# Performance work log

Measured on AMD Instinct MI355X. Metric: run time of the kernel, lower is better.

## Reference

```python
import jax, jax.numpy as jnp
import numpy as np
from jax import lax

SHARED = 512
THRESH = 1.0   # LifNeuron threshold from source
DECAY = 0.9    # assumed LIF membrane decay (LifNeuron source not provided)


def spike(u):
    return (u >= 0.0).astype(u.dtype)


def lif(x):
    # Leaky integrate-and-fire over the time axis. x: (B, T, D) -> spikes (B, T, D)
    def step(mem, xt):
        mem = DECAY * mem + xt
        s = spike(mem - THRESH)
        return mem - s * THRESH, s
    x_t = jnp.swapaxes(x, 0, 1)  # (T, B, D)
    _, spikes = lax.scan(step, jnp.zeros((x.shape[0], x.shape[2]), x.dtype), x_t)
    return jnp.swapaxes(spikes, 0, 1)


def setup_inputs() -> dict:
    key = jax.random.key(0)
    ks = jax.random.split(key, 10)
    B, T, S = 2, 32, 64
    Dv, Da = 768, 512
    TENSOR_DIM = (SHARED + 1) ** 2  # 263169

    def lin_w(k, fan_in, fan_out):
        # torch.nn.Linear default init scale ~ 1/sqrt(fan_in)
        return (jax.random.normal(k, (fan_out, fan_in), jnp.float32)
                * np.float32(1.0 / np.sqrt(fan_in)))

    return {
        "vision": jax.random.uniform(ks[0], (B, T, S, Dv), jnp.float32),
        "audio": jax.random.uniform(ks[1], (B, T, S, Da), jnp.float32),
        "vw1": lin_w(ks[2], Dv, SHARED), "vb1": jnp.zeros((SHARED,), jnp.float32),
        "vw2": lin_w(ks[3], SHARED, SHARED), "vb2": jnp.zeros((SHARED,), jnp.float32),
        "aw1": lin_w(ks[4], Da, SHARED), "ab1": jnp.zeros((SHARED,), jnp.float32),
        "aw2": lin_w(ks[5], SHARED, SHARED), "ab2": jnp.zeros((SHARED,), jnp.float32),
        "fw1": lin_w(ks[6], TENSOR_DIM, 2 * SHARED), "fb1": jnp.zeros((2 * SHARED,), jnp.float32),
        "fw2": lin_w(ks[7], 2 * SHARED, SHARED), "fb2": jnp.zeros((SHARED,), jnp.float32),
    }


def reference(vision, audio, vw1, vb1, vw2, vb2, aw1, ab1, aw2, ab2,
              fw1, fb1, fw2, fb2):
    def unimodal(x, w1, b1, w2, b2):
        p = x.mean(axis=2)  # (B, T, D_mod) - pool over spike/token axis
        h = jax.nn.relu(jnp.einsum('btd,hd->bth', p, w1) + b1)
        h = jnp.einsum('bth,oh->bto', h, w2) + b2  # (B, T, SHARED)
        ones = jnp.ones(h.shape[:-1] + (1,), h.dtype)
        return jnp.concatenate([h, ones], axis=-1)  # (B, T, SHARED+1)

    a = unimodal(vision, vw1, vb1, vw2, vb2)
    b = unimodal(audio, aw1, ab1, aw2, ab2)
    B, T, _ = a.shape
    # outer-product tensor fusion: (B, T, (SHARED+1)^2)
    tp = jnp.einsum('btd,bte->btde', a, b).reshape(B, T, -1)
    h = jax.nn.relu(jnp.einsum('btk,ok->bto', tp, fw1) + fb1)
    fused = jnp.einsum('bto,fo->btf', h, fw2) + fb2  # (B, T, SHARED)
    return lif(fused)
```

## Files before the change

kernel.cpp:

```cpp
#include <hip/hip_runtime.h>

#define AB 513
#define TD 263169

typedef float f4 __attribute__((ext_vector_type(4)));
typedef float f32x4 __attribute__((ext_vector_type(4)));
typedef short bf16x8 __attribute__((ext_vector_type(8)));
typedef int i32x4 __attribute__((ext_vector_type(4)));
#define GAS __attribute__((address_space(1)))
#define LAS __attribute__((address_space(3)))

__global__ __launch_bounds__(256) void pool_kernel(
    const float* __restrict__ vx, const float* __restrict__ ax,
    float* __restrict__ pvT, float* __restrict__ paT)
{
    int b = blockIdx.x;
    const float* x; float* pT; int D, bt, dc;
    if (b < 192) { x = vx; pT = pvT; D = 768; bt = b / 3; dc = b % 3; }
    else { b -= 192; x = ax; pT = paT; D = 512; bt = b >> 1; dc = b & 1; }
    const int d = dc * 256 + threadIdx.x;
    const float* xp = x + (size_t)bt * 64 * D + d;
    float s0 = 0.f, s1 = 0.f, s2 = 0.f, s3 = 0.f;
    #pragma unroll 4
    for (int ss = 0; ss < 64; ss += 4) {
        s0 += xp[(size_t)ss * D];
        s1 += xp[(size_t)(ss + 1) * D];
        s2 += xp[(size_t)(ss + 2) * D];
        s3 += xp[(size_t)(ss + 3) * D];
    }
    pT[d * 64 + bt] = ((s0 + s1) + (s2 + s3)) * 0.015625f;
}

__global__ __launch_bounds__(512) void mlp1_kernel(
    const float* __restrict__ pvT, const float* __restrict__ paT,
    const float* __restrict__ vw1, const float* __restrict__ vb1,
    const float* __restrict__ aw1, const float* __restrict__ ab1,
    float* __restrict__ h1vT, float* __restrict__ h1aT)
{
    const int isA = (blockIdx.x >= 64);
    const int D = isA ? 512 : 768;
    const float* pT = isA ? paT : pvT;
    const float* w1 = isA ? aw1 : vw1;
    const float* b1 = isA ? ab1 : vb1;
    float* h1T = isA ? h1aT : h1vT;
    const int tid = threadIdx.x, lane = tid & 63, w = tid >> 6;
    const int h = (blockIdx.x & 63) * 8 + w;
    const float* wr = w1 + (size_t)h * D;

    float a0 = 0.f, a1 = 0.f, a2 = 0.f, a3 = 0.f;
    for (int d = 0; d < D; d += 16) {
        const f4 w0 = *(const f4*)(wr + d);
        const f4 w1v = *(const f4*)(wr + d + 4);
        const f4 w2v = *(const f4*)(wr + d + 8);
        const f4 w3v = *(const f4*)(wr + d + 12);
        #pragma unroll
        for (int q = 0; q < 4; ++q) {
            a0 = fmaf(w0[q],  pT[(d + q) * 64 + lane], a0);
            a1 = fmaf(w1v[q], pT[(d + 4 + q) * 64 + lane], a1);
            a2 = fmaf(w2v[q], pT[(d + 8 + q) * 64 + lane], a2);
            a3 = fmaf(w3v[q], pT[(d + 12 + q) * 64 + lane], a3);
        }
    }
    h1T[h * 64 + lane] = fmaxf((a0 + a1) + (a2 + a3) + b1[h], 0.f);
}

__global__ __launch_bounds__(512) void mlp2_kernel(
    const float* __restrict__ h1vT, const float* __restrict__ h1aT,
    const float* __restrict__ vw2, const float* __restrict__ vb2,
    const float* __restrict__ aw2, const float* __restrict__ ab2,
    float* __restrict__ aTout, float* __restrict__ bTout)
{
    const int isA = (blockIdx.x >= 64);
    const float* hT = isA ? h1aT : h1vT;
    const float* w2 = isA ? aw2 : vw2;
    const float* b2 = isA ? ab2 : vb2;
    float* outT = isA ? bTout : aTout;
    const int tid = threadIdx.x, lane = tid & 63, w = tid >> 6;
    const int h = (blockIdx.x & 63) * 8 + w;
    const float* wr = w2 + (size_t)h * 512;

    float a0 = 0.f, a1 = 0.f, a2 = 0.f, a3 = 0.f;
    for (int d = 0; d < 512; d += 16) {
        const f4 w0 = *(const f4*)(wr + d);
        const f4 w1v = *(const f4*)(wr + d + 4);
        const f4 w2v = *(const f4*)(wr + d + 8);
        const f4 w3v = *(const f4*)(wr + d + 12);
        #pragma unroll
        for (int q = 0; q < 4; ++q) {
            a0 = fmaf(w0[q],  hT[(d + q) * 64 + lane], a0);
            a1 = fmaf(w1v[q], hT[(d + 4 + q) * 64 + lane], a1);
            a2 = fmaf(w2v[q], hT[(d + 8 + q) * 64 + lane], a2);
            a3 = fmaf(w3v[q], hT[(d + 12 + q) * 64 + lane], a3);
        }
    }
    outT[h * 64 + lane] = (a0 + a1) + (a2 + a3) + b2[h];
    if ((blockIdx.x & 63) == 0 && tid < 64) outT[512 * 64 + tid] = 1.0f;
}

__global__ __launch_bounds__(256) void aprep_kernel(
    const float* __restrict__ aT,
    short* __restrict__ aFc)
{
    const int t = blockIdx.x * 256 + threadIdx.x;
    const int l = t & 63, mt = (t >> 6) & 3, kt = t >> 8;
    const int m = mt * 16 + (l & 15);
    const int kbase = kt * 32 + ((l >> 4) << 3);
    const int cb = kt * 12 + mt * 3;
    #pragma unroll
    for (int i = 0; i < 8; ++i) {
        const float v = aT[(size_t)(kbase + i) * 64 + m];
        const unsigned u = __float_as_uint(v);
        const float r1 = v - __uint_as_float(u & 0xFFFF0000u);
        const unsigned u1 = __float_as_uint(r1);
        const float r2 = r1 - __uint_as_float(u1 & 0xFFFF0000u);
        const unsigned u2 = __float_as_uint(r2);
        aFc[((size_t)(cb + 0) * 64 + l) * 8 + i] = (short)(u >> 16);
        aFc[((size_t)(cb + 1) * 64 + l) * 8 + i] = (short)(u1 >> 16);
        aFc[((size_t)(cb + 2) * 64 + l) * 8 + i] = (short)(u2 >> 16);
    }
}

__global__ __launch_bounds__(512, 1) void bilinear_kernel(
    const float* __restrict__ fw1,
    const float* __restrict__ fb1,
    const float* __restrict__ aT,
    const float* __restrict__ bT,
    const short* __restrict__ aFc,
    float* __restrict__ hbufT)
{
    __shared__ float wring[3][8192];
    __shared__ short aring[3][6144];
    __shared__ float adump[256];

    const int tid = threadIdx.x;
    const int l = tid & 63, w = tid >> 6;
    const int o = blockIdx.x;
    const float* __restrict__ W = fw1 + (size_t)o * TD;
    const int lq = l >> 4, ln = l & 15;

    #define STAGE_W(e_)                                                        \
        do {                                                                   \
            const int ee_ = (e_), kt_ = ee_ >> 1, eh_ = ee_ & 1, en_ = ee_ % 3;\
            _Pragma("unroll")                                                  \
            for (int rr_ = 0; rr_ < 4; ++rr_) {                                \
                const int r_ = w * 4 + rr_;                                    \
                __builtin_amdgcn_global_load_lds(                              \
                    (const GAS unsigned*)(const void*)(W + (size_t)(kt_ * 32 + r_) * AB + 256 * eh_ + l * 4), \
                    (LAS unsigned*)(void*)(&wring[en_][r_ * 256]), 16, 0, 0);  \
            }                                                                  \
        } while (0)

    #define STAGE_A(kt_)                                                       \
        do {                                                                   \
            const int kk_ = (kt_), en_ = kk_ % 3;                              \
            const int c0_ = (w < 4) ? (2 * w) : (4 + w);                       \
            const short* s0_ = aFc + ((size_t)kk_ * 12 + c0_) * 512;           \
            __builtin_amdgcn_global_load_lds(                                  \
                (const GAS unsigned*)(const void*)(s0_ + l * 8),               \
                (LAS unsigned*)(void*)(&aring[en_][c0_ * 512]), 16, 0, 0);     \
            if (w < 4) {                                                       \
                const int c1_ = 2 * w + 1;                                     \
                const short* s1_ = aFc + ((size_t)kk_ * 12 + c1_) * 512;       \
                __builtin_amdgcn_global_load_lds(                              \
                    (const GAS unsigned*)(const void*)(s1_ + l * 8),           \
                    (LAS unsigned*)(void*)(&aring[en_][c1_ * 512]), 16, 0, 0); \
            } else {                                                           \
                const short* s1_ = aFc + (size_t)kk_ * 12 * 512;               \
                __builtin_amdgcn_global_load_lds(                              \
                    (const GAS unsigned*)(const void*)(s1_ + l * 2),           \
                    (LAS unsigned*)(void*)(adump), 4, 0, 0);                   \
            }                                                                  \
        } while (0)

    #define LOADA_LDS(kt_)                                                     \
        do {                                                                   \
            const int en_ = (kt_) % 3;                                         \
            _Pragma("unroll")                                                  \
            for (int mt_ = 0; mt_ < 4; ++mt_) {                                \
                A1[mt_] = *(const bf16x8*)&aring[en_][(mt_ * 3 + 0) * 512 + l * 8]; \
                A2[mt_] = *(const bf16x8*)&aring[en_][(mt_ * 3 + 1) * 512 + l * 8]; \
                A3[mt_] = *(const bf16x8*)&aring[en_][(mt_ * 3 + 2) * 512 + l * 8]; \
            }                                                                  \
        } while (0)

    #define COMPUTE(e_, EHC)                                                   \
        do {                                                                   \
            const float* __restrict__ wb_ = &wring[(e_) % 3][0];               \
            _Pragma("unroll")                                                  \
            for (int ntl = 0; ntl < 2; ++ntl) {                                \
                const int col_ = 32 * w + 16 * ntl + ln;                       \
                unsigned u0[8], u1[8], u2[8];                                  \
                _Pragma("unroll")                                              \
                for (int i = 0; i < 8; ++i) {                                  \
                    const float v = wb_[(lq * 8 + i) * 256 + col_];            \
                    u0[i] = __float_as_uint(v);                                \
                    const float r1 = v - __uint_as_float(u0[i] & 0xFFFF0000u); \
                    u1[i] = __float_as_uint(r1);                               \
                    const float r2 = r1 - __uint_as_float(u1[i] & 0xFFFF0000u);\
                    u2[i] = __float_as_uint(r2);                               \
                }                                                              \
                i32x4 p1, p2, p3;                                              \
                _Pragma("unroll")                                              \
                for (int j = 0; j < 4; ++j) {                                  \
                    p1[j] = (int)((u0[2 * j + 1] & 0xFFFF0000u) | (u0[2 * j] >> 16)); \
                    p2[j] = (int)((u1[2 * j + 1] & 0xFFFF0000u) | (u1[2 * j] >> 16)); \
                    p3[j] = (int)((u2[2 * j + 1] & 0xFFFF0000u) | (u2[2 * j] >> 16)); \
                }                                                              \
                const bf16x8 B1 = __builtin_bit_cast(bf16x8, p1);              \
                const bf16x8 B2 = __builtin_bit_cast(bf16x8, p2);              \
                const bf16x8 B3 = __builtin_bit_cast(bf16x8, p3);              \
                _Pragma("unroll")                                              \
                for (int mt = 0; mt < 4; ++mt) {                               \
                    acc[mt][(EHC) * 2 + ntl] = __builtin_amdgcn_mfma_f32_16x16x32_bf16(A1[mt], B1, acc[mt][(EHC) * 2 + ntl], 0, 0, 0); \
                    acc[mt][(EHC) * 2 + ntl] = __builtin_amdgcn_mfma_f32_16x16x32_bf16(A1[mt], B2, acc[mt][(EHC) * 2 + ntl], 0, 0, 0); \
                    acc[mt][(EHC) * 2 + ntl] = __builtin_amdgcn_mfma_f32_16x16x32_bf16(A2[mt], B1, acc[mt][(EHC) * 2 + ntl], 0, 0, 0); \
                    acc[mt][(EHC) * 2 + ntl] = __builtin_amdgcn_mfma_f32_16x16x32_bf16(A2[mt], B2, acc[mt][(EHC) * 2 + ntl], 0, 0, 0); \
                    acc[mt][(EHC) * 2 + ntl] = __builtin_amdgcn_mfma_f32_16x16x32_bf16(A1[mt], B3, acc[mt][(EHC) * 2 + ntl], 0, 0, 0); \
                    acc[mt][(EHC) * 2 + ntl] = __builtin_amdgcn_mfma_f32_16x16x32_bf16(A3[mt], B1, acc[mt][(EHC) * 2 + ntl], 0, 0, 0); \
                }                                                              \
            }                                                                  \
        } while (0)

    f32x4 acc[4][4];
    #pragma unroll
    for (int mt = 0; mt < 4; ++mt)
        #pragma unroll
        for (int nt = 0; nt < 4; ++nt)
            acc[mt][nt] = (f32x4){0.f, 0.f, 0.f, 0.f};
    bf16x8 A1[4], A2[4], A3[4];

    STAGE_W(0);
    STAGE_A(0);
    STAGE_W(1);
    STAGE_A(1);

    #pragma unroll 1
    for (int kt = 0; kt < 16; ++kt) {
        const int e0 = 2 * kt;
        asm volatile("s_waitcnt vmcnt(6)" ::: "memory");
        __builtin_amdgcn_s_barrier();
        LOADA_LDS(kt);
        COMPUTE(e0, 0);
        __builtin_amdgcn_s_barrier();
        STAGE_W(e0 + 2 <= 31 ? e0 + 2 : 31);
        STAGE_A(kt + 2 <= 15 ? kt + 2 : 15);
        asm volatile("s_waitcnt vmcnt(6)" ::: "memory");
        __builtin_amdgcn_s_barrier();
        COMPUTE(e0 + 1, 1);
        __builtin_amdgcn_s_barrier();
        STAGE_W(e0 + 3 <= 31 ? e0 + 3 : 31);
    }
    asm volatile("s_waitcnt vmcnt(0)" ::: "memory");
    __builtin_amdgcn_s_barrier();

    float ysum[4][4];
    #pragma unroll
    for (int mt = 0; mt < 4; ++mt)
        #pragma unroll
        for (int r = 0; r < 4; ++r) ysum[mt][r] = 0.f;
    #pragma unroll
    for (int mt = 0; mt < 4; ++mt) {
        const int bt0 = mt * 16 + lq * 4;
        #pragma unroll
        for (int ntg = 0; ntg < 4; ++ntg) {
            const int e = 256 * (ntg >> 1) + 32 * w + 16 * (ntg & 1) + ln;
            const f4 bv = *(const f4*)(bT + (size_t)e * 64 + bt0);
            #pragma unroll
            for (int r = 0; r < 4; ++r)
                ysum[mt][r] = fmaf(acc[mt][ntg][r], bv[r], ysum[mt][r]);
        }
    }
    #pragma unroll
    for (int mt = 0; mt < 4; ++mt)
        #pragma unroll
        for (int r = 0; r < 4; ++r) {
            float v = ysum[mt][r];
            v += __shfl_xor(v, 1, 64);
            v += __shfl_xor(v, 2, 64);
            v += __shfl_xor(v, 4, 64);
            v += __shfl_xor(v, 8, 64);
            ysum[mt][r] = v;
        }
    if (ln == 0) {
        #pragma unroll
        for (int mt = 0; mt < 4; ++mt)
            #pragma unroll
            for (int r = 0; r < 4; ++r)
                wring[0][w * 64 + mt * 16 + lq * 4 + r] = ysum[mt][r];
    }

    {
        const int we0 = w * 64;
        float s0 = 0.f, s1 = 0.f, s2 = 0.f, s3 = 0.f;
        #pragma unroll 4
        for (int k = 0; k < 64; k += 4) {
            s0 = fmaf(aT[(size_t)(we0 + k) * 64 + l], W[(size_t)(we0 + k) * AB + 512], s0);
            s1 = fmaf(aT[(size_t)(we0 + k + 1) * 64 + l], W[(size_t)(we0 + k + 1) * AB + 512], s1);
            s2 = fmaf(aT[(size_t)(we0 + k + 2) * 64 + l], W[(size_t)(we0 + k + 2) * AB + 512], s2);
            s3 = fmaf(aT[(size_t)(we0 + k + 3) * 64 + l], W[(size_t)(we0 + k + 3) * AB + 512], s3);
        }
        #pragma unroll 4
        for (int k = 0; k < 64; k += 4) {
            s0 = fmaf(W[(size_t)512 * AB + we0 + k], bT[(size_t)(we0 + k) * 64 + l], s0);
            s1 = fmaf(W[(size_t)512 * AB + we0 + k + 1], bT[(size_t)(we0 + k + 1) * 64 + l], s1);
            s2 = fmaf(W[(size_t)512 * AB + we0 + k + 2], bT[(size_t)(we0 + k + 2) * 64 + l], s2);
            s3 = fmaf(W[(size_t)512 * AB + we0 + k + 3], bT[(size_t)(we0 + k + 3) * 64 + l], s3);
        }
        wring[0][512 + w * 64 + l] = (s0 + s1) + (s2 + s3);
    }

    __syncthreads();

    if (w == 0) {
        float t2 = 0.f;
        #pragma unroll
        for (int k = 0; k < 8; ++k)
            t2 += wring[0][k * 64 + l] + wring[0][512 + k * 64 + l];
        t2 += W[(size_t)512 * AB + 512] + fb1[o];
        hbufT[(size_t)o * 64 + l] = fmaxf(t2, 0.f);
    }
    #undef STAGE_W
    #undef STAGE_A
    #undef LOADA_LDS
    #undef COMPUTE
}

__global__ __launch_bounds__(512) void fuse2_kernel(
    const float* __restrict__ hbufT,
    const float* __restrict__ fw2,
    const float* __restrict__ fb2,
    float* __restrict__ fused)
{
    const int tid = threadIdx.x, lane = tid & 63, w = tid >> 6;
    #pragma unroll
    for (int k = 0; k < 2; ++k) {
        const int f = blockIdx.x * 16 + w * 2 + k;
        const float* wr = fw2 + (size_t)f * 1024;
        float a0 = 0.f, a1 = 0.f, a2 = 0.f, a3 = 0.f;
        for (int o = 0; o < 1024; o += 16) {
            const f4 w0 = *(const f4*)(wr + o);
            const f4 w1v = *(const f4*)(wr + o + 4);
            const f4 w2v = *(const f4*)(wr + o + 8);
            const f4 w3v = *(const f4*)(wr + o + 12);
            #pragma unroll
            for (int q = 0; q < 4; ++q) {
                a0 = fmaf(w0[q],  hbufT[(o + q) * 64 + lane], a0);
                a1 = fmaf(w1v[q], hbufT[(o + 4 + q) * 64 + lane], a1);
                a2 = fmaf(w2v[q], hbufT[(o + 8 + q) * 64 + lane], a2);
                a3 = fmaf(w3v[q], hbufT[(o + 12 + q) * 64 + lane], a3);
            }
        }
        fused[lane * 512 + f] = (a0 + a1) + (a2 + a3) + fb2[f];
    }
}

__global__ __launch_bounds__(256) void lif_kernel(
    const float* __restrict__ fused,
    float* __restrict__ out)
{
    const int idx = blockIdx.x * 256 + threadIdx.x;
    if (idx >= 1024) return;
    const int b = idx >> 9, dd = idx & 511;
    float mem = 0.f;
    for (int t = 0; t < 32; ++t) {
        const size_t off = ((size_t)(b * 32 + t) * 512) + dd;
        mem = 0.9f * mem + fused[off];
        const float s = (mem >= 1.0f) ? 1.0f : 0.0f;
        out[off] = s;
        mem -= s;
    }
}

extern "C" void kernel_launch(void* const* d_in, const int* in_sizes, int n_in,
                              void* d_out, int out_size, void* d_ws, size_t ws_size,
                              hipStream_t stream) {
    const float* vision = (const float*)d_in[0];
    const float* audio  = (const float*)d_in[1];
    const float* vw1 = (const float*)d_in[2];
    const float* vb1 = (const float*)d_in[3];
    const float* vw2 = (const float*)d_in[4];
    const float* vb2 = (const float*)d_in[5];
    const float* aw1 = (const float*)d_in[6];
    const float* ab1 = (const float*)d_in[7];
    const float* aw2 = (const float*)d_in[8];
    const float* ab2 = (const float*)d_in[9];
    const float* fw1 = (const float*)d_in[10];
    const float* fb1 = (const float*)d_in[11];
    const float* fw2 = (const float*)d_in[12];
    const float* fb2 = (const float*)d_in[13];
    float* out = (float*)d_out;

    float* ws    = (float*)d_ws;
    float* pvT   = ws;
    float* paT   = pvT + 768 * 64;
    float* h1vT  = paT + 512 * 64;
    float* h1aT  = h1vT + 512 * 64;
    float* aT    = h1aT + 512 * 64;
    float* bT    = aT + AB * 64;
    float* hbufT = bT + AB * 64;
    float* fused = hbufT + 1024 * 64;
    short* aFc   = (short*)(fused + 64 * 512);

    pool_kernel<<<320, 256, 0, stream>>>(vision, audio, pvT, paT);
    mlp1_kernel<<<128, 512, 0, stream>>>(pvT, paT, vw1, vb1, aw1, ab1, h1vT, h1aT);
    mlp2_kernel<<<128, 512, 0, stream>>>(h1vT, h1aT, vw2, vb2, aw2, ab2, aT, bT);
    aprep_kernel<<<16, 256, 0, stream>>>(aT, aFc);
    bilinear_kernel<<<1024, 512, 0, stream>>>(fw1, fb1, aT, bT, aFc, hbufT);
    fuse2_kernel<<<32, 512, 0, stream>>>(hbufT, fw2, fb2, fused);
    lif_kernel<<<4, 256, 0, stream>>>(fused, out);
}
```

Before: 440.8 us.

## Swap bilinear GEMM operand roles and load fw1 directly into registers

The bilinear kernel now treats the fw1 rows as the MFMA A operand and the precomputed bf16-split b vectors as B, instead of the reverse. Each wave loads its own 64 rows of fw1 straight from global memory into registers with a two-register double buffer. This replaces the LDS ring, global_load_lds staging and barriers. The final contraction with a also folds in the column-512 weight term. The change removes LDS traffic and barrier synchronisation, but the fw1 reads are now strided row accesses (8 floats per lane across rows of stride 513), which may coalesce poorly, and register pressure rises.

```diff
diff --git a/kernel.cpp b/kernel.cpp
--- a/kernel.cpp
+++ b/kernel.cpp
@@ -7,8 +7,6 @@
 typedef float f32x4 __attribute__((ext_vector_type(4)));
 typedef short bf16x8 __attribute__((ext_vector_type(8)));
 typedef int i32x4 __attribute__((ext_vector_type(4)));
-#define GAS __attribute__((address_space(1)))
-#define LAS __attribute__((address_space(3)))
 
 __global__ __launch_bounds__(256) void pool_kernel(
     const float* __restrict__ vx, const float* __restrict__ ax,
@@ -97,26 +95,26 @@
     if ((blockIdx.x & 63) == 0 && tid < 64) outT[512 * 64 + tid] = 1.0f;
 }
 
-__global__ __launch_bounds__(256) void aprep_kernel(
-    const float* __restrict__ aT,
-    short* __restrict__ aFc)
+__global__ __launch_bounds__(256) void bprep_kernel(
+    const float* __restrict__ bT,
+    short* __restrict__ bF)
 {
     const int t = blockIdx.x * 256 + threadIdx.x;
-    const int l = t & 63, mt = (t >> 6) & 3, kt = t >> 8;
-    const int m = mt * 16 + (l & 15);
-    const int kbase = kt * 32 + ((l >> 4) << 3);
-    const int cb = kt * 12 + mt * 3;
+    const int l = t & 63, frag = t >> 6;
+    const int kt = frag / 12, rem = frag % 12;
+    const int nt = rem / 3, lvl = rem % 3;
+    const int bt = nt * 16 + (l & 15);
+    const int ebase = kt * 32 + ((l >> 4) << 3);
     #pragma unroll
     for (int i = 0; i < 8; ++i) {
-        const float v = aT[(size_t)(kbase + i) * 64 + m];
+        const float v = bT[(size_t)(ebase + i) * 64 + bt];
         const unsigned u = __float_as_uint(v);
         const float r1 = v - __uint_as_float(u & 0xFFFF0000u);
         const unsigned u1 = __float_as_uint(r1);
         const float r2 = r1 - __uint_as_float(u1 & 0xFFFF0000u);
         const unsigned u2 = __float_as_uint(r2);
-        aFc[((size_t)(cb + 0) * 64 + l) * 8 + i] = (short)(u >> 16);
-        aFc[((size_t)(cb + 1) * 64 + l) * 8 + i] = (short)(u1 >> 16);
-        aFc[((size_t)(cb + 2) * 64 + l) * 8 + i] = (short)(u2 >> 16);
+        const unsigned sel = (lvl == 0) ? u : (lvl == 1) ? u1 : u2;
+        bF[(size_t)frag * 512 + l * 8 + i] = (short)(sel >> 16);
     }
 }
 
@@ -125,74 +123,48 @@
     const float* __restrict__ fb1,
     const float* __restrict__ aT,
     const float* __restrict__ bT,
-    const short* __restrict__ aFc,
+    const short* __restrict__ bF,
     float* __restrict__ hbufT)
 {
-    __shared__ float wring[3][8192];
-    __shared__ short aring[3][6144];
-    __shared__ float adump[256];
+    __shared__ float red[8][64];
+    __shared__ float redB[8][64];
 
     const int tid = threadIdx.x;
     const int l = tid & 63, w = tid >> 6;
     const int o = blockIdx.x;
     const float* __restrict__ W = fw1 + (size_t)o * TD;
-    const int lq = l >> 4, ln = l & 15;
-
-    #define STAGE_W(e_)                                                        \
+    const int ln = l & 15, lq = l >> 4;
+
+    #define WLOAD(W0r, W1r, kt_)                                               \
         do {                                                                   \
-            const int ee_ = (e_), kt_ = ee_ >> 1, eh_ = ee_ & 1, en_ = ee_ % 3;\
             _Pragma("unroll")                                                  \
-            for (int rr_ = 0; rr_ < 4; ++rr_) {                                \
-                const int r_ = w * 4 + rr_;                                    \
-                __builtin_amdgcn_global_load_lds(                              \
-                    (const GAS unsigned*)(const void*)(W + (size_t)(kt_ * 32 + r_) * AB + 256 * eh_ + l * 4), \
-                    (LAS unsigned*)(void*)(&wring[en_][r_ * 256]), 16, 0, 0);  \
+            for (int mt_ = 0; mt_ < 4; ++mt_) {                                \
+                const float* p_ = W + (size_t)((w * 4 + mt_) * 16 + ln) * AB   \
+                                    + (kt_) * 32 + lq * 8;                     \
+                W0r[mt_] = *(const f4*)p_;                                     \
+                W1r[mt_] = *(const f4*)(p_ + 4);                               \
             }                                                                  \
         } while (0)
 
-    #define STAGE_A(kt_)                                                       \
+    #define BLOAD(kt_)                                                         \
         do {                                                                   \
-            const int kk_ = (kt_), en_ = kk_ % 3;                              \
-            const int c0_ = (w < 4) ? (2 * w) : (4 + w);                       \
-            const short* s0_ = aFc + ((size_t)kk_ * 12 + c0_) * 512;           \
-            __builtin_amdgcn_global_load_lds(                                  \
-                (const GAS unsigned*)(const void*)(s0_ + l * 8),               \
-                (LAS unsigned*)(void*)(&aring[en_][c0_ * 512]), 16, 0, 0);     \
-            if (w < 4) {                                                       \
-                const int c1_ = 2 * w + 1;                                     \
-                const short* s1_ = aFc + ((size_t)kk_ * 12 + c1_) * 512;       \
-                __builtin_amdgcn_global_load_lds(                              \
-                    (const GAS unsigned*)(const void*)(s1_ + l * 8),           \
-                    (LAS unsigned*)(void*)(&aring[en_][c1_ * 512]), 16, 0, 0); \
-            } else {                                                           \
-                const short* s1_ = aFc + (size_t)kk_ * 12 * 512;               \
-                __builtin_amdgcn_global_load_lds(                              \
-                    (const GAS unsigned*)(const void*)(s1_ + l * 2),           \
-                    (LAS unsigned*)(void*)(adump), 4, 0, 0);                   \
+            _Pragma("unroll")                                                  \
+            for (int nt_ = 0; nt_ < 4; ++nt_) {                                \
+                const short* q_ = bF + (size_t)(((kt_) * 4 + nt_) * 3) * 512 + l * 8; \
+                B1[nt_] = *(const bf16x8*)(q_);                                \
+                B2[nt_] = *(const bf16x8*)(q_ + 512);                          \
+                B3[nt_] = *(const bf16x8*)(q_ + 1024);                         \
             }                                                                  \
         } while (0)
 
-    #define LOADA_LDS(kt_)                                                     \
+    #define COMPUTE(W0r, W1r)                                                  \
         do {                                                                   \
-            const int en_ = (kt_) % 3;                                         \
             _Pragma("unroll")                                                  \
-            for (int mt_ = 0; mt_ < 4; ++mt_) {                                \
-                A1[mt_] = *(const bf16x8*)&aring[en_][(mt_ * 3 + 0) * 512 + l * 8]; \
-                A2[mt_] = *(const bf16x8*)&aring[en_][(mt_ * 3 + 1) * 512 + l * 8]; \
-                A3[mt_] = *(const bf16x8*)&aring[en_][(mt_ * 3 + 2) * 512 + l * 8]; \
-            }                                                                  \
-        } while (0)
-
-    #define COMPUTE(e_, EHC)                                                   \
-        do {                                                                   \
-            const float* __restrict__ wb_ = &wring[(e_) % 3][0];               \
-            _Pragma("unroll")                                                  \
-            for (int ntl = 0; ntl < 2; ++ntl) {                                \
-                const int col_ = 32 * w + 16 * ntl + ln;                       \
+            for (int mt = 0; mt < 4; ++mt) {                                   \
                 unsigned u0[8], u1[8], u2[8];                                  \
                 _Pragma("unroll")                                              \
                 for (int i = 0; i < 8; ++i) {                                  \
-                    const float v = wb_[(lq * 8 + i) * 256 + col_];            \
+                    const float v = (i < 4) ? W0r[mt][i] : W1r[mt][i - 4];     \
                     u0[i] = __float_as_uint(v);                                \
                     const float r1 = v - __uint_as_float(u0[i] & 0xFFFF0000u); \
                     u1[i] = __float_as_uint(r1);                               \
@@ -206,17 +178,17 @@
                     p2[j] = (int)((u1[2 * j + 1] & 0xFFFF0000u) | (u1[2 * j] >> 16)); \
                     p3[j] = (int)((u2[2 * j + 1] & 0xFFFF0000u) | (u2[2 * j] >> 16)); \
                 }                                                              \
-                const bf16x8 B1 = __builtin_bit_cast(bf16x8, p1);              \
-                const bf16x8 B2 = __builtin_bit_cast(bf16x8, p2);              \
-                const bf16x8 B3 = __builtin_bit_cast(bf16x8, p3);              \
+                const bf16x8 A1 = __builtin_bit_cast(bf16x8, p1);              \
+                const bf16x8 A2 = __builtin_bit_cast(bf16x8, p2);              \
+                const bf16x8 A3 = __builtin_bit_cast(bf16x8, p3);              \
                 _Pragma("unroll")                                              \
-                for (int mt = 0; mt < 4; ++mt) {                               \
-                    acc[mt][(EHC) * 2 + ntl] = __builtin_amdgcn_mfma_f32_16x16x32_bf16(A1[mt], B1, acc[mt][(EHC) * 2 + ntl], 0, 0, 0); \
-                    acc[mt][(EHC) * 2 + ntl] = __builtin_amdgcn_mfma_f32_16x16x32_bf16(A1[mt], B2, acc[mt][(EHC) * 2 + ntl], 0, 0, 0); \
-                    acc[mt][(EHC) * 2 + ntl] = __builtin_amdgcn_mfma_f32_16x16x32_bf16(A2[mt], B1, acc[mt][(EHC) * 2 + ntl], 0, 0, 0); \
-                    acc[mt][(EHC) * 2 + ntl] = __builtin_amdgcn_mfma_f32_16x16x32_bf16(A2[mt], B2, acc[mt][(EHC) * 2 + ntl], 0, 0, 0); \
-                    acc[mt][(EHC) * 2 + ntl] = __builtin_amdgcn_mfma_f32_16x16x32_bf16(A1[mt], B3, acc[mt][(EHC) * 2 + ntl], 0, 0, 0); \
-                    acc[mt][(EHC) * 2 + ntl] = __builtin_amdgcn_mfma_f32_16x16x32_bf16(A3[mt], B1, acc[mt][(EHC) * 2 + ntl], 0, 0, 0); \
+                for (int nt = 0; nt < 4; ++nt) {                               \
+                    acc[mt][nt] = __builtin_amdgcn_mfma_f32_16x16x32_bf16(A1, B1[nt], acc[mt][nt], 0, 0, 0); \
+                    acc[mt][nt] = __builtin_amdgcn_mfma_f32_16x16x32_bf16(A1, B2[nt], acc[mt][nt], 0, 0, 0); \
+                    acc[mt][nt] = __builtin_amdgcn_mfma_f32_16x16x32_bf16(A2, B1[nt], acc[mt][nt], 0, 0, 0); \
+                    acc[mt][nt] = __builtin_amdgcn_mfma_f32_16x16x32_bf16(A2, B2[nt], acc[mt][nt], 0, 0, 0); \
+                    acc[mt][nt] = __builtin_amdgcn_mfma_f32_16x16x32_bf16(A1, B3[nt], acc[mt][nt], 0, 0, 0); \
+                    acc[mt][nt] = __builtin_amdgcn_mfma_f32_16x16x32_bf16(A3, B1[nt], acc[mt][nt], 0, 0, 0); \
                 }                                                              \
             }                                                                  \
         } while (0)
@@ -227,86 +199,65 @@
         #pragma unroll
         for (int nt = 0; nt < 4; ++nt)
             acc[mt][nt] = (f32x4){0.f, 0.f, 0.f, 0.f};
-    bf16x8 A1[4], A2[4], A3[4];
-
-    STAGE_W(0);
-    STAGE_A(0);
-    STAGE_W(1);
-    STAGE_A(1);
+
+    f4 Wa0[4], Wa1[4], Wb0[4], Wb1[4];
+    bf16x8 B1[4], B2[4], B3[4];
+
+    WLOAD(Wa0, Wa1, 0);
 
     #pragma unroll 1
-    for (int kt = 0; kt < 16; ++kt) {
-        const int e0 = 2 * kt;
-        asm volatile("s_waitcnt vmcnt(6)" ::: "memory");
-        __builtin_amdgcn_s_barrier();
-        LOADA_LDS(kt);
-        COMPUTE(e0, 0);
-        __builtin_amdgcn_s_barrier();
-        STAGE_W(e0 + 2 <= 31 ? e0 + 2 : 31);
-        STAGE_A(kt + 2 <= 15 ? kt + 2 : 15);
-        asm volatile("s_waitcnt vmcnt(6)" ::: "memory");
-        __builtin_amdgcn_s_barrier();
-        COMPUTE(e0 + 1, 1);
-        __builtin_amdgcn_s_barrier();
-        STAGE_W(e0 + 3 <= 31 ? e0 + 3 : 31);
-    }
-    asm volatile("s_waitcnt vmcnt(0)" ::: "memory");
-    __builtin_amdgcn_s_barrier();
-
-    float ysum[4][4];
-    #pragma unroll
-    for (int mt = 0; mt < 4; ++mt)
-        #pragma unroll
-        for (int r = 0; r < 4; ++r) ysum[mt][r] = 0.f;
+    for (int it = 0; it < 7; ++it) {
+        const int kt = 2 * it;
+        WLOAD(Wb0, Wb1, kt + 1);
+        BLOAD(kt);
+        COMPUTE(Wa0, Wa1);
+        WLOAD(Wa0, Wa1, kt + 2);
+        BLOAD(kt + 1);
+        COMPUTE(Wb0, Wb1);
+    }
+    WLOAD(Wb0, Wb1, 15);
+    BLOAD(14);
+    COMPUTE(Wa0, Wa1);
+    BLOAD(15);
+    COMPUTE(Wb0, Wb1);
+
+    float y[4] = {0.f, 0.f, 0.f, 0.f};
     #pragma unroll
     for (int mt = 0; mt < 4; ++mt) {
-        const int bt0 = mt * 16 + lq * 4;
-        #pragma unroll
-        for (int ntg = 0; ntg < 4; ++ntg) {
-            const int e = 256 * (ntg >> 1) + 32 * w + 16 * (ntg & 1) + ln;
-            const f4 bv = *(const f4*)(bT + (size_t)e * 64 + bt0);
+        #pragma unroll
+        for (int r = 0; r < 4; ++r) {
+            const int d = 64 * w + mt * 16 + lq * 4 + r;
+            const float wc = W[(size_t)d * AB + 512];
             #pragma unroll
-            for (int r = 0; r < 4; ++r)
-                ysum[mt][r] = fmaf(acc[mt][ntg][r], bv[r], ysum[mt][r]);
-        }
-    }
-    #pragma unroll
-    for (int mt = 0; mt < 4; ++mt)
-        #pragma unroll
-        for (int r = 0; r < 4; ++r) {
-            float v = ysum[mt][r];
-            v += __shfl_xor(v, 1, 64);
-            v += __shfl_xor(v, 2, 64);
-            v += __shfl_xor(v, 4, 64);
-            v += __shfl_xor(v, 8, 64);
-            ysum[mt][r] = v;
-        }
-    if (ln == 0) {
-        #pragma unroll
-        for (int mt = 0; mt < 4; ++mt)
-            #pragma unroll
-            for (int r = 0; r < 4; ++r)
-                wring[0][w * 64 + mt * 16 + lq * 4 + r] = ysum[mt][r];
+            for (int nt = 0; nt < 4; ++nt) {
+                const float av = aT[(size_t)d * 64 + nt * 16 + ln];
+                y[nt] = fmaf(av, acc[mt][nt][r] + wc, y[nt]);
+            }
+        }
+    }
+    #pragma unroll
+    for (int nt = 0; nt < 4; ++nt) {
+        float v = y[nt];
+        v += __shfl_xor(v, 16, 64);
+        v += __shfl_xor(v, 32, 64);
+        y[nt] = v;
+    }
+    if (lq == 0) {
+        #pragma unroll
+        for (int nt = 0; nt < 4; ++nt) red[w][nt * 16 + ln] = y[nt];
     }
 
     {
-        const int we0 = w * 64;
         float s0 = 0.f, s1 = 0.f, s2 = 0.f, s3 = 0.f;
+        const int e0 = 64 * w;
         #pragma unroll 4
         for (int k = 0; k < 64; k += 4) {
-            s0 = fmaf(aT[(size_t)(we0 + k) * 64 + l], W[(size_t)(we0 + k) * AB + 512], s0);
-            s1 = fmaf(aT[(size_t)(we0 + k + 1) * 64 + l], W[(size_t)(we0 + k + 1) * AB + 512], s1);
-            s2 = fmaf(aT[(size_t)(we0 + k + 2) * 64 + l], W[(size_t)(we0 + k + 2) * AB + 512], s2);
-            s3 = fmaf(aT[(size_t)(we0 + k + 3) * 64 + l], W[(size_t)(we0 + k + 3) * AB + 512], s3);
-        }
-        #pragma unroll 4
-        for (int k = 0; k < 64; k += 4) {
-            s0 = fmaf(W[(size_t)512 * AB + we0 + k], bT[(size_t)(we0 + k) * 64 + l], s0);
-            s1 = fmaf(W[(size_t)512 * AB + we0 + k + 1], bT[(size_t)(we0 + k + 1) * 64 + l], s1);
-            s2 = fmaf(W[(size_t)512 * AB + we0 + k + 2], bT[(size_t)(we0 + k + 2) * 64 + l], s2);
-            s3 = fmaf(W[(size_t)512 * AB + we0 + k + 3], bT[(size_t)(we0 + k + 3) * 64 + l], s3);
-        }
-        wring[0][512 + w * 64 + l] = (s0 + s1) + (s2 + s3);
+            s0 = fmaf(W[(size_t)512 * AB + e0 + k], bT[(size_t)(e0 + k) * 64 + l], s0);
+            s1 = fmaf(W[(size_t)512 * AB + e0 + k + 1], bT[(size_t)(e0 + k + 1) * 64 + l], s1);
+            s2 = fmaf(W[(size_t)512 * AB + e0 + k + 2], bT[(size_t)(e0 + k + 2) * 64 + l], s2);
+            s3 = fmaf(W[(size_t)512 * AB + e0 + k + 3], bT[(size_t)(e0 + k + 3) * 64 + l], s3);
+        }
+        redB[w][l] = (s0 + s1) + (s2 + s3);
     }
 
     __syncthreads();
@@ -314,14 +265,12 @@
     if (w == 0) {
         float t2 = 0.f;
         #pragma unroll
-        for (int k = 0; k < 8; ++k)
-            t2 += wring[0][k * 64 + l] + wring[0][512 + k * 64 + l];
+        for (int k = 0; k < 8; ++k) t2 += red[k][l] + redB[k][l];
         t2 += W[(size_t)512 * AB + 512] + fb1[o];
         hbufT[(size_t)o * 64 + l] = fmaxf(t2, 0.f);
     }
-    #undef STAGE_W
-    #undef STAGE_A
-    #undef LOADA_LDS
+    #undef WLOAD
+    #undef BLOAD
     #undef COMPUTE
 }
 
@@ -399,13 +348,13 @@
     float* bT    = aT + AB * 64;
     float* hbufT = bT + AB * 64;
     float* fused = hbufT + 1024 * 64;
-    short* aFc   = (short*)(fused + 64 * 512);
+    short* bF    = (short*)(fused + 64 * 512);
 
     pool_kernel<<<320, 256, 0, stream>>>(vision, audio, pvT, paT);
     mlp1_kernel<<<128, 512, 0, stream>>>(pvT, paT, vw1, vb1, aw1, ab1, h1vT, h1aT);
     mlp2_kernel<<<128, 512, 0, stream>>>(h1vT, h1aT, vw2, vb2, aw2, ab2, aT, bT);
-    aprep_kernel<<<16, 256, 0, stream>>>(aT, aFc);
-    bilinear_kernel<<<1024, 512, 0, stream>>>(fw1, fb1, aT, bT, aFc, hbufT);
+    bprep_kernel<<<48, 256, 0, stream>>>(bT, bF);
+    bilinear_kernel<<<1024, 512, 0, stream>>>(fw1, fb1, aT, bT, bF, hbufT);
     fuse2_kernel<<<32, 512, 0, stream>>>(hbufT, fw2, fb2, fused);
     lif_kernel<<<4, 256, 0, stream>>>(fused, out);
 }
```

New measurement: 469.3 us. +6.5%, slower.

## Process four output rows per bilinear block and split edge terms into aux kernel

Applied to the files above, without the earlier changes.

The bilinear kernel now handles four output neurons per block (256 blocks instead of 1024), running one continuous software pipeline across all four so weight and A-fragment prefetch carries over between outputs instead of restarting per block. The row/column edge terms of the 513x513 weight (the ones-column contributions) plus bias move into a separate aux_kernel that writes a per-output partial sum the main kernel adds in its epilogue. This is meant to remove per-block pipeline prologue/drain and the strided tail loads from the hot kernel. In exchange it adds an extra kernel launch that re-reads strided weight columns, and with only 256 blocks some CUs may sit idle.

```diff
diff --git a/kernel.cpp b/kernel.cpp
--- a/kernel.cpp
+++ b/kernel.cpp
@@ -120,72 +120,103 @@
     }
 }
 
+__global__ __launch_bounds__(512) void aux_kernel(
+    const float* __restrict__ fw1, const float* __restrict__ fb1,
+    const float* __restrict__ aT, const float* __restrict__ bT,
+    float* __restrict__ aux)
+{
+    __shared__ float wc[513], wr[512], r8[8][64];
+    const int o = blockIdx.x, tid = threadIdx.x;
+    const int l = tid & 63, w = tid >> 6;
+    const float* __restrict__ W = fw1 + (size_t)o * TD;
+    wc[tid] = W[(size_t)tid * AB + 512];
+    if (tid == 0) wc[512] = W[(size_t)512 * AB + 512];
+    wr[tid] = W[(size_t)512 * AB + tid];
+    __syncthreads();
+    float s = 0.f;
+    for (int i = w; i < 513; i += 8) {
+        s = fmaf(wc[i], aT[(size_t)i * 64 + l], s);
+        if (i < 512) s = fmaf(wr[i], bT[(size_t)i * 64 + l], s);
+    }
+    r8[w][l] = s;
+    __syncthreads();
+    if (w == 0) {
+        float t = fb1[o];
+        #pragma unroll
+        for (int k = 0; k < 8; ++k) t += r8[k][l];
+        aux[(size_t)o * 64 + l] = t;
+    }
+}
+
 __global__ __launch_bounds__(512, 1) void bilinear_kernel(
     const float* __restrict__ fw1,
-    const float* __restrict__ fb1,
-    const float* __restrict__ aT,
     const float* __restrict__ bT,
     const short* __restrict__ aFc,
+    const float* __restrict__ aux,
     float* __restrict__ hbufT)
 {
     __shared__ float wring[3][8192];
     __shared__ short aring[3][6144];
     __shared__ float adump[256];
+    __shared__ float red[8][64];
 
     const int tid = threadIdx.x;
     const int l = tid & 63, w = tid >> 6;
-    const int o = blockIdx.x;
-    const float* __restrict__ W = fw1 + (size_t)o * TD;
+    const int o0 = blockIdx.x * 4;
     const int lq = l >> 4, ln = l & 15;
 
-    #define STAGE_W(e_)                                                        \
-        do {                                                                   \
-            const int ee_ = (e_), kt_ = ee_ >> 1, eh_ = ee_ & 1, en_ = ee_ % 3;\
+    #define SW(gg_)                                                            \
+        do {                                                                   \
+            const int G_ = (gg_);                                              \
+            const int oo_ = o0 + (G_ >> 5);                                    \
+            const int kq_ = (G_ >> 1) & 15, eh_ = G_ & 1, sl_ = G_ % 3;        \
+            const float* base_ = fw1 + (size_t)oo_ * TD                        \
+                + (size_t)(kq_ * 32) * AB + 256 * eh_ + l * 4;                 \
             _Pragma("unroll")                                                  \
             for (int rr_ = 0; rr_ < 4; ++rr_) {                                \
                 const int r_ = w * 4 + rr_;                                    \
                 __builtin_amdgcn_global_load_lds(                              \
-                    (const GAS unsigned*)(const void*)(W + (size_t)(kt_ * 32 + r_) * AB + 256 * eh_ + l * 4), \
-                    (LAS unsigned*)(void*)(&wring[en_][r_ * 256]), 16, 0, 0);  \
-            }                                                                  \
-        } while (0)
-
-    #define STAGE_A(kt_)                                                       \
-        do {                                                                   \
-            const int kk_ = (kt_), en_ = kk_ % 3;                              \
+                    (const GAS unsigned*)(const void*)(base_ + (size_t)r_ * AB), \
+                    (LAS unsigned*)(void*)(&wring[sl_][r_ * 256]), 16, 0, 0);  \
+            }                                                                  \
+        } while (0)
+
+    #define SA(gg_)                                                            \
+        do {                                                                   \
+            const int gk_ = (gg_);                                             \
+            const int c_ = gk_ & 15, sl_ = gk_ % 3;                            \
             const int c0_ = (w < 4) ? (2 * w) : (4 + w);                       \
-            const short* s0_ = aFc + ((size_t)kk_ * 12 + c0_) * 512;           \
+            const short* s0_ = aFc + ((size_t)c_ * 12 + c0_) * 512;            \
             __builtin_amdgcn_global_load_lds(                                  \
                 (const GAS unsigned*)(const void*)(s0_ + l * 8),               \
-                (LAS unsigned*)(void*)(&aring[en_][c0_ * 512]), 16, 0, 0);     \
+                (LAS unsigned*)(void*)(&aring[sl_][c0_ * 512]), 16, 0, 0);     \
             if (w < 4) {                                                       \
                 const int c1_ = 2 * w + 1;                                     \
-                const short* s1_ = aFc + ((size_t)kk_ * 12 + c1_) * 512;       \
+                const short* s1_ = aFc + ((size_t)c_ * 12 + c1_) * 512;        \
                 __builtin_amdgcn_global_load_lds(                              \
                     (const GAS unsigned*)(const void*)(s1_ + l * 8),           \
-                    (LAS unsigned*)(void*)(&aring[en_][c1_ * 512]), 16, 0, 0); \
+                    (LAS unsigned*)(void*)(&aring[sl_][c1_ * 512]), 16, 0, 0); \
             } else {                                                           \
-                const short* s1_ = aFc + (size_t)kk_ * 12 * 512;               \
                 __builtin_amdgcn_global_load_lds(                              \
-                    (const GAS unsigned*)(const void*)(s1_ + l * 2),           \
+                    (const GAS unsigned*)(const void*)(aFc + (size_t)c_ * 12 * 512 + l * 2), \
                     (LAS unsigned*)(void*)(adump), 4, 0, 0);                   \
             }                                                                  \
         } while (0)
 
-    #define LOADA_LDS(kt_)                                                     \
-        do {                                                                   \
-            const int en_ = (kt_) % 3;                                         \
+    #define LA(gg_)                                                            \
+        do {                                                                   \
+            const int sl_ = (gg_) % 3;                                         \
             _Pragma("unroll")                                                  \
             for (int mt_ = 0; mt_ < 4; ++mt_) {                                \
-                A1[mt_] = *(const bf16x8*)&aring[en_][(mt_ * 3 + 0) * 512 + l * 8]; \
-                A2[mt_] = *(const bf16x8*)&aring[en_][(mt_ * 3 + 1) * 512 + l * 8]; \
-                A3[mt_] = *(const bf16x8*)&aring[en_][(mt_ * 3 + 2) * 512 + l * 8]; \
-            }                                                                  \
-        } while (0)
-
-    #define COMPUTE(e_, EHC)                                                   \
-        do {                                                                   \
-            const float* __restrict__ wb_ = &wring[(e_) % 3][0];               \
+                A1[mt_] = *(const bf16x8*)&aring[sl_][(mt_ * 3 + 0) * 512 + l * 8]; \
+                A2[mt_] = *(const bf16x8*)&aring[sl_][(mt_ * 3 + 1) * 512 + l * 8]; \
+                A3[mt_] = *(const bf16x8*)&aring[sl_][(mt_ * 3 + 2) * 512 + l * 8]; \
+            }                                                                  \
+        } while (0)
+
+    #define COMPUTE(gg_, EHC)                                                  \
+        do {                                                                   \
+            const float* __restrict__ wb_ = &wring[(gg_) % 3][0];              \
             _Pragma("unroll")                                                  \
             for (int ntl = 0; ntl < 2; ++ntl) {                                \
                 const int col_ = 32 * w + 16 * ntl + ln;                       \
@@ -221,108 +252,116 @@
             }                                                                  \
         } while (0)
 
+    #define EPI(jj_)                                                           \
+        do {                                                                   \
+            float ysum[4][4];                                                  \
+            _Pragma("unroll")                                                  \
+            for (int mt = 0; mt < 4; ++mt)                                     \
+                _Pragma("unroll")                                              \
+                for (int r = 0; r < 4; ++r) ysum[mt][r] = 0.f;                 \
+            _Pragma("unroll")                                                  \
+            for (int mt = 0; mt < 4; ++mt)                                     \
+                _Pragma("unroll")                                              \
+                for (int ntg = 0; ntg < 4; ++ntg)                              \
+                    _Pragma("unroll")                                          \
+                    for (int r = 0; r < 4; ++r)                                \
+                        ysum[mt][r] = fmaf(acc[mt][ntg][r], bv[mt][ntg][r], ysum[mt][r]); \
+            _Pragma("unroll")                                                  \
+            for (int mt = 0; mt < 4; ++mt)                                     \
+                _Pragma("unroll")                                              \
+                for (int r = 0; r < 4; ++r) {                                  \
+                    float v = ysum[mt][r];                                     \
+                    v += __shfl_xor(v, 1, 64);                                 \
+                    v += __shfl_xor(v, 2, 64);                                 \
+                    v += __shfl_xor(v, 4, 64);                                 \
+                    v += __shfl_xor(v, 8, 64);                                 \
+                    ysum[mt][r] = v;                                           \
+                }                                                              \
+            if (ln == 0) {                                                     \
+                _Pragma("unroll")                                              \
+                for (int mt = 0; mt < 4; ++mt)                                 \
+                    _Pragma("unroll")                                          \
+                    for (int r = 0; r < 4; ++r)                                \
+                        red[w][mt * 16 + lq * 4 + r] = ysum[mt][r];            \
+            }                                                                  \
+            asm volatile("s_waitcnt lgkmcnt(0)" ::: "memory");                 \
+            __builtin_amdgcn_s_barrier();                                      \
+            if (w == 0) {                                                      \
+                float t2 = auxv[jj_];                                          \
+                _Pragma("unroll")                                              \
+                for (int k = 0; k < 8; ++k) t2 += red[k][l];                   \
+                res[jj_] = fmaxf(t2, 0.f);                                     \
+            }                                                                  \
+            __builtin_amdgcn_s_barrier();                                      \
+            _Pragma("unroll")                                                  \
+            for (int mt = 0; mt < 4; ++mt)                                     \
+                _Pragma("unroll")                                              \
+                for (int ntg = 0; ntg < 4; ++ntg)                              \
+                    acc[mt][ntg] = (f32x4){0.f, 0.f, 0.f, 0.f};                \
+        } while (0)
+
+    #define ODO(jj_)                                                           \
+        do {                                                                   \
+            _Pragma("unroll 1")                                                \
+            for (int kt = 0; kt < 16; ++kt) {                                  \
+                const int g = (jj_) * 32 + 2 * kt;                             \
+                const int gk = (jj_) * 16 + kt;                                \
+                asm volatile("s_waitcnt vmcnt(6)" ::: "memory");               \
+                __builtin_amdgcn_s_barrier();                                  \
+                LA(gk);                                                        \
+                COMPUTE(g, 0);                                                 \
+                __builtin_amdgcn_s_barrier();                                  \
+                { const int t1 = (g + 2 > 127) ? 127 : g + 2; SW(t1); }        \
+                { const int t2 = (gk + 2 > 63) ? 63 : gk + 2; SA(t2); }        \
+                asm volatile("s_waitcnt vmcnt(6)" ::: "memory");               \
+                __builtin_amdgcn_s_barrier();                                  \
+                COMPUTE(g + 1, 1);                                             \
+                __builtin_amdgcn_s_barrier();                                  \
+                { const int t3 = (g + 3 > 127) ? 127 : g + 3; SW(t3); }        \
+            }                                                                  \
+            EPI(jj_);                                                          \
+        } while (0)
+
     f32x4 acc[4][4];
     #pragma unroll
     for (int mt = 0; mt < 4; ++mt)
         #pragma unroll
-        for (int nt = 0; nt < 4; ++nt)
-            acc[mt][nt] = (f32x4){0.f, 0.f, 0.f, 0.f};
+        for (int ntg = 0; ntg < 4; ++ntg)
+            acc[mt][ntg] = (f32x4){0.f, 0.f, 0.f, 0.f};
     bf16x8 A1[4], A2[4], A3[4];
-
-    STAGE_W(0);
-    STAGE_A(0);
-    STAGE_W(1);
-    STAGE_A(1);
-
-    #pragma unroll 1
-    for (int kt = 0; kt < 16; ++kt) {
-        const int e0 = 2 * kt;
-        asm volatile("s_waitcnt vmcnt(6)" ::: "memory");
-        __builtin_amdgcn_s_barrier();
-        LOADA_LDS(kt);
-        COMPUTE(e0, 0);
-        __builtin_amdgcn_s_barrier();
-        STAGE_W(e0 + 2 <= 31 ? e0 + 2 : 31);
-        STAGE_A(kt + 2 <= 15 ? kt + 2 : 15);
-        asm volatile("s_waitcnt vmcnt(6)" ::: "memory");
-        __builtin_amdgcn_s_barrier();
-        COMPUTE(e0 + 1, 1);
-        __builtin_amdgcn_s_barrier();
-        STAGE_W(e0 + 3 <= 31 ? e0 + 3 : 31);
-    }
-    asm volatile("s_waitcnt vmcnt(0)" ::: "memory");
-    __builtin_amdgcn_s_barrier();
-
-    float ysum[4][4];
+    float res[4];
+
+    f4 bv[4][4];
     #pragma unroll
     for (int mt = 0; mt < 4; ++mt)
         #pragma unroll
-        for (int r = 0; r < 4; ++r) ysum[mt][r] = 0.f;
-    #pragma unroll
-    for (int mt = 0; mt < 4; ++mt) {
-        const int bt0 = mt * 16 + lq * 4;
-        #pragma unroll
         for (int ntg = 0; ntg < 4; ++ntg) {
             const int e = 256 * (ntg >> 1) + 32 * w + 16 * (ntg & 1) + ln;
-            const f4 bv = *(const f4*)(bT + (size_t)e * 64 + bt0);
-            #pragma unroll
-            for (int r = 0; r < 4; ++r)
-                ysum[mt][r] = fmaf(acc[mt][ntg][r], bv[r], ysum[mt][r]);
+            bv[mt][ntg] = *(const f4*)(bT + (size_t)e * 64 + mt * 16 + lq * 4);
         }
-    }
+    float auxv[4];
     #pragma unroll
-    for (int mt = 0; mt < 4; ++mt)
-        #pragma unroll
-        for (int r = 0; r < 4; ++r) {
-            float v = ysum[mt][r];
-            v += __shfl_xor(v, 1, 64);
-            v += __shfl_xor(v, 2, 64);
-            v += __shfl_xor(v, 4, 64);
-            v += __shfl_xor(v, 8, 64);
-            ysum[mt][r] = v;
-        }
-    if (ln == 0) {
-        #pragma unroll
-        for (int mt = 0; mt < 4; ++mt)
-            #pragma unroll
-            for (int r = 0; r < 4; ++r)
-                wring[0][w * 64 + mt * 16 + lq * 4 + r] = ysum[mt][r];
-    }
-
-    {
-        const int we0 = w * 64;
-        float s0 = 0.f, s1 = 0.f, s2 = 0.f, s3 = 0.f;
-        #pragma unroll 4
-        for (int k = 0; k < 64; k += 4) {
-            s0 = fmaf(aT[(size_t)(we0 + k) * 64 + l], W[(size_t)(we0 + k) * AB + 512], s0);
-            s1 = fmaf(aT[(size_t)(we0 + k + 1) * 64 + l], W[(size_t)(we0 + k + 1) * AB + 512], s1);
-            s2 = fmaf(aT[(size_t)(we0 + k + 2) * 64 + l], W[(size_t)(we0 + k + 2) * AB + 512], s2);
-            s3 = fmaf(aT[(size_t)(we0 + k + 3) * 64 + l], W[(size_t)(we0 + k + 3) * AB + 512], s3);
-        }
-        #pragma unroll 4
-        for (int k = 0; k < 64; k += 4) {
-            s0 = fmaf(W[(size_t)512 * AB + we0 + k], bT[(size_t)(we0 + k) * 64 + l], s0);
-            s1 = fmaf(W[(size_t)512 * AB + we0 + k + 1], bT[(size_t)(we0 + k + 1) * 64 + l], s1);
-            s2 = fmaf(W[(size_t)512 * AB + we0 + k + 2], bT[(size_t)(we0 + k + 2) * 64 + l], s2);
-            s3 = fmaf(W[(size_t)512 * AB + we0 + k + 3], bT[(size_t)(we0 + k + 3) * 64 + l], s3);
-        }
-        wring[0][512 + w * 64 + l] = (s0 + s1) + (s2 + s3);
-    }
-
-    __syncthreads();
-
+    for (int jj = 0; jj < 4; ++jj) auxv[jj] = aux[(size_t)(o0 + jj) * 64 + l];
+
+    SW(0); SA(0); SW(1); SA(1);
+
+    ODO(0);
+    ODO(1);
+    ODO(2);
+    ODO(3);
+
+    asm volatile("s_waitcnt vmcnt(0)" ::: "memory");
     if (w == 0) {
-        float t2 = 0.f;
-        #pragma unroll
-        for (int k = 0; k < 8; ++k)
-            t2 += wring[0][k * 64 + l] + wring[0][512 + k * 64 + l];
-        t2 += W[(size_t)512 * AB + 512] + fb1[o];
-        hbufT[(size_t)o * 64 + l] = fmaxf(t2, 0.f);
-    }
-    #undef STAGE_W
-    #undef STAGE_A
-    #undef LOADA_LDS
+        #pragma unroll
+        for (int jj = 0; jj < 4; ++jj)
+            hbufT[(size_t)(o0 + jj) * 64 + l] = res[jj];
+    }
+    #undef SW
+    #undef SA
+    #undef LA
     #undef COMPUTE
+    #undef EPI
+    #undef ODO
 }
 
 __global__ __launch_bounds__(512) void fuse2_kernel(
@@ -400,12 +439,14 @@
     float* hbufT = bT + AB * 64;
     float* fused = hbufT + 1024 * 64;
     short* aFc   = (short*)(fused + 64 * 512);
+    float* aux   = (float*)(aFc + 98304);
 
     pool_kernel<<<320, 256, 0, stream>>>(vision, audio, pvT, paT);
     mlp1_kernel<<<128, 512, 0, stream>>>(pvT, paT, vw1, vb1, aw1, ab1, h1vT, h1aT);
     mlp2_kernel<<<128, 512, 0, stream>>>(h1vT, h1aT, vw2, vb2, aw2, ab2, aT, bT);
     aprep_kernel<<<16, 256, 0, stream>>>(aT, aFc);
-    bilinear_kernel<<<1024, 512, 0, stream>>>(fw1, fb1, aT, bT, aFc, hbufT);
+    aux_kernel<<<1024, 512, 0, stream>>>(fw1, fb1, aT, bT, aux);
+    bilinear_kernel<<<256, 512, 0, stream>>>(fw1, bT, aFc, aux, hbufT);
     fuse2_kernel<<<32, 512, 0, stream>>>(hbufT, fw2, fb2, fused);
     lif_kernel<<<4, 256, 0, stream>>>(fused, out);
 }
```

Result: slower. 456.9 us (+3.6%).
